# Kernel tuning notes

Hardware: AMD Instinct MI355X
Metric: run time of the kernel (lower is better)

Reference implementation:

```python
import jax, jax.numpy as jnp
import numpy as np

K = 512
DIM = 256
BETA = 0.25


def setup_inputs() -> dict:
    key = jax.random.key(0)
    k1, k2 = jax.random.split(key)
    x = jax.random.normal(k1, (64, DIM, 32, 32), dtype=jnp.float32)
    lookup_table = jax.random.normal(k2, (K, DIM), dtype=jnp.float32)
    return {"x": x, "lookup_table": lookup_table}


def reference(x, lookup_table):
    b, d, h, w = x.shape
    # [b,d,h,w] -> [b*h*w, d]
    xf = jnp.transpose(x, (0, 2, 3, 1)).reshape(-1, d)
    # Squared Euclidean distances (argmin identical to torch.cdist argmin)
    d2 = (
        jnp.sum(xf * xf, axis=-1, keepdims=True)
        - 2.0 * (xf @ lookup_table.T)
        + jnp.sum(lookup_table * lookup_table, axis=-1)
    )  # [N, K]
    q = jnp.argmin(d2, axis=1)  # [N]
    x_e = lookup_table[q].reshape(b, h, w, d).transpose(0, 3, 1, 2)  # [b,d,h,w]
    q_x = q.reshape(b, h, w)
    codebook_loss = jnp.mean(jnp.square(jax.lax.stop_gradient(x) - x_e))
    commitment_loss = jnp.mean(jnp.square(x - jax.lax.stop_gradient(x_e)))
    loss = codebook_loss + BETA * commitment_loss
    return x_e, q_x, loss
```

## Files before the change

kernel.cpp:

```cpp
#include <hip/hip_runtime.h>

#define DIM     256
#define HW      1024
#define N_ROWS  65536
#define NT      512
#define QBM     128
#define NBLK    512
#define MARGIN  0.0625f

#define OUT_Q_OFF    16777216
#define OUT_LOSS_OFF 16842752

#define WS_DIST   512
#define WS_X2     1024
#define WS_CNT_I  1536
#define WS_LIST_I 2048
#define WS_LUTBF_B 524288

typedef __attribute__((ext_vector_type(8))) short short8v;
typedef __attribute__((ext_vector_type(4))) float floatx4;

__device__ __forceinline__ unsigned short bf16_rne(float f) {
    unsigned int u = __float_as_uint(f);
    u += 0x7fffu + ((u >> 16) & 1u);
    return (unsigned short)(u >> 16);
}
__device__ __forceinline__ float bf16_to_f(unsigned short h) {
    return __uint_as_float(((unsigned int)h) << 16);
}
__device__ __forceinline__ uint4 pack8(const unsigned short* h) {
    uint4 u;
    u.x = (unsigned)h[0] | ((unsigned)h[1] << 16);
    u.y = (unsigned)h[2] | ((unsigned)h[3] << 16);
    u.z = (unsigned)h[4] | ((unsigned)h[5] << 16);
    u.w = (unsigned)h[6] | ((unsigned)h[7] << 16);
    return u;
}

__global__ void c2_kernel(const float* __restrict__ lut, float* __restrict__ ws) {
    if (threadIdx.x == 0) ((int*)ws)[WS_CNT_I] = 0;
    int t = threadIdx.x;
    for (int k = t; k < 512; k += 256) {
        const float4* row = (const float4*)(lut + (size_t)k * DIM);
        float s = 0.f;
        #pragma unroll 8
        for (int i = 0; i < DIM / 4; ++i) {
            float4 v = row[i];
            s += v.x * v.x + v.y * v.y + v.z * v.z + v.w * v.w;
        }
        ws[k] = s;
    }
}

__global__ void lutprep_kernel(const float* __restrict__ lut, float* __restrict__ ws) {
    int g = blockIdx.x * 256 + threadIdx.x;
    int lane = g & 63;
    int ctg  = (g >> 6) & 31;
    int dcg  = g >> 11;
    int code = ctg * 16 + (lane & 15);
    int d0   = dcg * 32 + (lane >> 4) * 8;
    const float* src = lut + (size_t)code * DIM + d0;
    unsigned short hi[8], lo[8];
    #pragma unroll
    for (int j = 0; j < 8; ++j) {
        float v = src[j];
        unsigned short h = bf16_rne(v);
        hi[j] = h;
        lo[j] = bf16_rne(v - bf16_to_f(h));
    }
    char* dst = (char*)ws + WS_LUTBF_B + (size_t)((dcg * 32 + ctg) * 2) * 1024 + lane * 16;
    *(uint4*)dst          = pack8(hi);
    *(uint4*)(dst + 1024) = pack8(lo);
}

__global__ __launch_bounds__(NT, 2) void vq_kernel(const float* __restrict__ x,
                                                   const float* __restrict__ lut,
                                                   float* __restrict__ out,
                                                   float* __restrict__ ws) {
    __shared__ char aS[2][16384];
    __shared__ float c2s[512];
    __shared__ float redv1[4][QBM];
    __shared__ float redv2[4][QBM];
    __shared__ int   redi1[4][QBM];
    __shared__ int   qsh[QBM];
    __shared__ float wsumd[2];
    __shared__ float wsumx[8];

    const char* lutbf = (const char*)ws + WS_LUTBF_B;

    const int tid = threadIdx.x;
    const int blk = blockIdx.x;
    const int n0  = blk * QBM;
    const int b   = n0 >> 10;
    const int hw0 = n0 & 1023;
    const float* xb = x + (size_t)b * (DIM * HW) + hw0;

    for (int k = tid; k < 512; k += NT) c2s[k] = ws[k];

    const int wave = tid >> 6;
    const int lane = tid & 63;
    const int l15  = lane & 15;
    const int l4   = lane >> 4;
    const int rg   = wave >> 2;
    const int cg   = wave & 3;

    const int srow   = tid & 127;
    const int schunk = tid >> 7;
    const int srt    = srow >> 4;
    const int slf    = schunk * 16 + (srow & 15);
    char* awr_hi0 = &aS[0][srt * 1024 + slf * 16];
    char* awr_hi1 = &aS[1][srt * 1024 + slf * 16];

    float x2local = 0.f;
    floatx4 acc[4][8];
    #pragma unroll
    for (int i = 0; i < 4; ++i)
        #pragma unroll
        for (int j = 0; j < 8; ++j) acc[i][j] = (floatx4)0.f;

    {
        const float* src = xb + (size_t)(schunk * 8) * HW + srow;
        unsigned short hi[8], lo[8];
        #pragma unroll
        for (int j = 0; j < 8; ++j) {
            float v = src[(size_t)j * HW];
            x2local = fmaf(v, v, x2local);
            unsigned short h = bf16_rne(v);
            hi[j] = h;
            lo[j] = bf16_rne(v - bf16_to_f(h));
        }
        *(uint4*)awr_hi0          = pack8(hi);
        *(uint4*)(awr_hi0 + 8192) = pack8(lo);
    }
    __syncthreads();

    for (int dc = 0; dc < 8; ++dc) {
        const int cur = dc & 1;
        float xn[8];
        if (dc < 7) {
            const float* src = xb + (size_t)((dc + 1) * 32 + schunk * 8) * HW + srow;
            #pragma unroll
            for (int j = 0; j < 8; ++j) xn[j] = src[(size_t)j * HW];
        }
        short8v ah[4], al[4];
        #pragma unroll
        for (int rtl = 0; rtl < 4; ++rtl) {
            const char* ra = &aS[cur][(rg * 4 + rtl) * 1024 + lane * 16];
            ah[rtl] = *(const short8v*)ra;
            al[rtl] = *(const short8v*)(ra + 8192);
        }
        short8v bh[8], bl[8];
        #pragma unroll
        for (int ct = 0; ct < 8; ++ct) {
            const char* bp = lutbf + (size_t)((dc * 32 + cg * 8 + ct) * 2) * 1024 + lane * 16;
            bh[ct] = *(const short8v*)bp;
            bl[ct] = *(const short8v*)(bp + 1024);
        }
        #pragma unroll
        for (int ct = 0; ct < 8; ++ct) {
            #pragma unroll
            for (int rtl = 0; rtl < 4; ++rtl) {
                acc[rtl][ct] = __builtin_amdgcn_mfma_f32_16x16x32_bf16(ah[rtl], bh[ct], acc[rtl][ct], 0, 0, 0);
                acc[rtl][ct] = __builtin_amdgcn_mfma_f32_16x16x32_bf16(al[rtl], bh[ct], acc[rtl][ct], 0, 0, 0);
                acc[rtl][ct] = __builtin_amdgcn_mfma_f32_16x16x32_bf16(ah[rtl], bl[ct], acc[rtl][ct], 0, 0, 0);
            }
        }
        if (dc < 7) {
            unsigned short hi[8], lo[8];
            #pragma unroll
            for (int j = 0; j < 8; ++j) {
                float v = xn[j];
                x2local = fmaf(v, v, x2local);
                unsigned short h = bf16_rne(v);
                hi[j] = h;
                lo[j] = bf16_rne(v - bf16_to_f(h));
            }
            char* wr = cur ? awr_hi0 : awr_hi1;
            *(uint4*)wr          = pack8(hi);
            *(uint4*)(wr + 8192) = pack8(lo);
            __syncthreads();
        }
    }

    #pragma unroll
    for (int rtl = 0; rtl < 4; ++rtl) {
        #pragma unroll
        for (int r = 0; r < 4; ++r) {
            float v1 = 3.4e38f, v2 = 3.4e38f; int i1 = 0;
            #pragma unroll
            for (int ct = 0; ct < 8; ++ct) {
                int code = cg * 128 + ct * 16 + l15;
                float dist = fmaf(-2.f, acc[rtl][ct][r], c2s[code]);
                if (dist < v1) { v2 = v1; v1 = dist; i1 = code; }
                else if (dist < v2) v2 = dist;
            }
            #pragma unroll
            for (int off = 1; off < 16; off <<= 1) {
                float ov1 = __shfl_xor(v1, off, 64);
                int   oi1 = __shfl_xor(i1, off, 64);
                float ov2 = __shfl_xor(v2, off, 64);
                float nv2 = fminf(fmaxf(v1, ov1), fminf(v2, ov2));
                if (ov1 < v1 || (ov1 == v1 && oi1 < i1)) { v1 = ov1; i1 = oi1; }
                v2 = nv2;
            }
            if (l15 == 0) {
                int row = rg * 64 + rtl * 16 + l4 * 4 + r;
                redv1[cg][row] = v1; redi1[cg][row] = i1; redv2[cg][row] = v2;
            }
        }
    }
    __syncthreads();

    float dist_part = 0.f;
    if (tid < QBM) {
        const int row = tid;
        float v1 = redv1[0][row]; int i1 = redi1[0][row]; float v2 = redv2[0][row];
        #pragma unroll
        for (int s = 1; s < 4; ++s) {
            float ov1 = redv1[s][row]; int oi1 = redi1[s][row]; float ov2 = redv2[s][row];
            float nv2 = fminf(fmaxf(v1, ov1), fminf(v2, ov2));
            if (ov1 < v1 || (ov1 == v1 && oi1 < i1)) { v1 = ov1; i1 = oi1; }
            v2 = nv2;
        }
        qsh[row] = i1;
        out[OUT_Q_OFF + n0 + row] = (float)i1;
        if (v2 - v1 <= MARGIN) {
            int idx = atomicAdd((int*)ws + WS_CNT_I, 1);
            ((int*)ws)[WS_LIST_I + idx] = n0 + row;
        }
        dist_part = v1;
    }

    float dv = dist_part;
    #pragma unroll
    for (int off = 32; off; off >>= 1) dv += __shfl_down(dv, off, 64);
    if (lane == 0 && wave < 2) wsumd[wave] = dv;
    float xv = x2local;
    #pragma unroll
    for (int off = 32; off; off >>= 1) xv += __shfl_down(xv, off, 64);
    if (lane == 0) wsumx[wave] = xv;
    __syncthreads();
    if (tid == 0) {
        float xs = 0.f;
        #pragma unroll
        for (int w = 0; w < 8; ++w) xs += wsumx[w];
        ws[WS_DIST + blk] = wsumd[0] + wsumd[1];
        ws[WS_X2 + blk]   = xs;
    }

    {
        const int row = tid & 127;
        const int dg  = tid >> 7;
        const int q   = qsh[row];
        const float* crow = lut + (size_t)q * DIM;
        float* ob = out + (size_t)b * (DIM * HW) + hw0 + row;
        #pragma unroll 4
        for (int i = 0; i < 16; ++i) {
            int d0 = dg * 64 + i * 4;
            float4 c = *(const float4*)(crow + d0);
            ob[(size_t)(d0 + 0) * HW] = c.x;
            ob[(size_t)(d0 + 1) * HW] = c.y;
            ob[(size_t)(d0 + 2) * HW] = c.z;
            ob[(size_t)(d0 + 3) * HW] = c.w;
        }
    }
}

__global__ void exact_kernel(const float* __restrict__ x, const float* __restrict__ lut,
                             float* __restrict__ out, const float* __restrict__ ws) {
    __shared__ float xr[DIM];
    __shared__ float rv[256];
    __shared__ int   ri[256];
    const int cnt = ((const int*)ws)[WS_CNT_I];
    const int* list = (const int*)ws + WS_LIST_I;
    const int tid = threadIdx.x;
    for (int ii = blockIdx.x; ii < cnt; ii += gridDim.x) {
        const int row = list[ii];
        const int b = row >> 10, hw = row & 1023;
        __syncthreads();
        xr[tid] = x[(size_t)b * (DIM * HW) + (size_t)tid * HW + hw];
        __syncthreads();
        float bv = 3.4e38f; int bi = 0;
        #pragma unroll
        for (int k2 = 0; k2 < 2; ++k2) {
            int k = tid + k2 * 256;
            const float* cr = lut + (size_t)k * DIM;
            float dot = 0.f;
            for (int d = 0; d < DIM; ++d) dot = fmaf(xr[d], cr[d], dot);
            float dist = fmaf(-2.f, dot, ws[k]);
            if (dist < bv || (dist == bv && k < bi)) { bv = dist; bi = k; }
        }
        rv[tid] = bv; ri[tid] = bi;
        __syncthreads();
        for (int s = 128; s; s >>= 1) {
            if (tid < s) {
                float ov = rv[tid + s]; int oi = ri[tid + s];
                if (ov < rv[tid] || (ov == rv[tid] && oi < ri[tid])) {
                    rv[tid] = ov; ri[tid] = oi;
                }
            }
            __syncthreads();
        }
        const int q = ri[0];
        if (tid == 0) out[OUT_Q_OFF + row] = (float)q;
        out[(size_t)b * (DIM * HW) + (size_t)tid * HW + hw] = lut[(size_t)q * DIM + tid];
    }
}

__global__ void loss_kernel(float* __restrict__ out, const float* __restrict__ ws) {
    __shared__ float wsum[4];
    int tid = threadIdx.x;
    float s = 0.f;
    for (int i = tid; i < 1024; i += 256) s += ws[WS_DIST + i];
    #pragma unroll
    for (int off = 32; off; off >>= 1) s += __shfl_down(s, off, 64);
    if ((tid & 63) == 0) wsum[tid >> 6] = s;
    __syncthreads();
    if (tid == 0) {
        float total = wsum[0] + wsum[1] + wsum[2] + wsum[3];
        out[OUT_LOSS_OFF] = total * (1.25f / 16777216.f);
    }
}

extern "C" void kernel_launch(void* const* d_in, const int* in_sizes, int n_in,
                              void* d_out, int out_size, void* d_ws, size_t ws_size,
                              hipStream_t stream) {
    const float* x   = (const float*)d_in[0];
    const float* lut = (const float*)d_in[1];
    float* out = (float*)d_out;
    float* ws  = (float*)d_ws;

    c2_kernel<<<1, 256, 0, stream>>>(lut, ws);
    lutprep_kernel<<<64, 256, 0, stream>>>(lut, ws);
    vq_kernel<<<NBLK, NT, 0, stream>>>(x, lut, out, ws);
    exact_kernel<<<2048, 256, 0, stream>>>(x, lut, out, ws);
    loss_kernel<<<1, 256, 0, stream>>>(out, ws);
}
```

Baseline: 147.4 us.

## Stage bf16 codebook tiles in LDS via async global-to-LDS double buffering

The split hi/lo bf16 codebook slices are now copied into a double-buffered 64KB-per-stage LDS region with global_load_lds, prefetching the next d-chunk while the current one is consumed, instead of every wave reading its B fragments straight from global memory. The x tile drops to a single buffer guarded by an extra barrier. The codebook squared norms move from shared memory into registers, and the MFMA loop is reordered into three passes. The cost is 144KB of dynamic LDS per block, which likely allows only one block per CU despite launch bounds asking for two, so latency hiding from occupancy is traded for shared reuse of B across row groups.

Result: no change. 145.6 us (-1.2%).

```diff
diff --git a/kernel.cpp b/kernel.cpp
--- a/kernel.cpp
+++ b/kernel.cpp
@@ -17,8 +17,14 @@
 #define WS_LIST_I 2048
 #define WS_LUTBF_B 524288
 
+#define VQ_LDS (147456)
+
 typedef __attribute__((ext_vector_type(8))) short short8v;
 typedef __attribute__((ext_vector_type(4))) float floatx4;
+
+#define GLOAD_LDS16(gaddr, laddr) \
+    __builtin_amdgcn_global_load_lds((const __attribute__((address_space(1))) unsigned int*)(gaddr), \
+                                     (__attribute__((address_space(3))) unsigned int*)(laddr), 16, 0, 0)
 
 __device__ __forceinline__ unsigned short bf16_rne(float f) {
     unsigned int u = __float_as_uint(f);
@@ -77,14 +83,8 @@
                                                    const float* __restrict__ lut,
                                                    float* __restrict__ out,
                                                    float* __restrict__ ws) {
-    __shared__ char aS[2][16384];
-    __shared__ float c2s[512];
-    __shared__ float redv1[4][QBM];
-    __shared__ float redv2[4][QBM];
-    __shared__ int   redi1[4][QBM];
-    __shared__ int   qsh[QBM];
-    __shared__ float wsumd[2];
-    __shared__ float wsumx[8];
+    extern __shared__ char smem[];
+    char* abuf = smem + 131072;
 
     const char* lutbf = (const char*)ws + WS_LUTBF_B;
 
@@ -95,8 +95,6 @@
     const int hw0 = n0 & 1023;
     const float* xb = x + (size_t)b * (DIM * HW) + hw0;
 
-    for (int k = tid; k < 512; k += NT) c2s[k] = ws[k];
-
     const int wave = tid >> 6;
     const int lane = tid & 63;
     const int l15  = lane & 15;
@@ -104,12 +102,15 @@
     const int rg   = wave >> 2;
     const int cg   = wave & 3;
 
+    float c2reg[8];
+    #pragma unroll
+    for (int ct = 0; ct < 8; ++ct) c2reg[ct] = ws[cg * 128 + ct * 16 + l15];
+
     const int srow   = tid & 127;
     const int schunk = tid >> 7;
     const int srt    = srow >> 4;
     const int slf    = schunk * 16 + (srow & 15);
-    char* awr_hi0 = &aS[0][srt * 1024 + slf * 16];
-    char* awr_hi1 = &aS[1][srt * 1024 + slf * 16];
+    char* awr = abuf + srt * 1024 + slf * 16;
 
     float x2local = 0.f;
     floatx4 acc[4][8];
@@ -119,6 +120,11 @@
         for (int j = 0; j < 8; ++j) acc[i][j] = (floatx4)0.f;
 
     {
+        #pragma unroll
+        for (int c = 0; c < 8; ++c) {
+            int u = c * 8 + wave;
+            GLOAD_LDS16(lutbf + (size_t)u * 1024 + lane * 16, smem + u * 1024);
+        }
         const float* src = xb + (size_t)(schunk * 8) * HW + srow;
         unsigned short hi[8], lo[8];
         #pragma unroll
@@ -129,15 +135,23 @@
             hi[j] = h;
             lo[j] = bf16_rne(v - bf16_to_f(h));
         }
-        *(uint4*)awr_hi0          = pack8(hi);
-        *(uint4*)(awr_hi0 + 8192) = pack8(lo);
+        *(uint4*)awr          = pack8(hi);
+        *(uint4*)(awr + 8192) = pack8(lo);
     }
     __syncthreads();
 
     for (int dc = 0; dc < 8; ++dc) {
         const int cur = dc & 1;
+        char* bcur = smem + cur * 65536;
         float xn[8];
         if (dc < 7) {
+            char* bnxt = smem + (cur ^ 1) * 65536;
+            const char* bsrc = lutbf + (size_t)(dc + 1) * 65536;
+            #pragma unroll
+            for (int c = 0; c < 8; ++c) {
+                int u = c * 8 + wave;
+                GLOAD_LDS16(bsrc + (size_t)u * 1024 + lane * 16, bnxt + u * 1024);
+            }
             const float* src = xb + (size_t)((dc + 1) * 32 + schunk * 8) * HW + srow;
             #pragma unroll
             for (int j = 0; j < 8; ++j) xn[j] = src[(size_t)j * HW];
@@ -145,27 +159,34 @@
         short8v ah[4], al[4];
         #pragma unroll
         for (int rtl = 0; rtl < 4; ++rtl) {
-            const char* ra = &aS[cur][(rg * 4 + rtl) * 1024 + lane * 16];
+            const char* ra = abuf + (rg * 4 + rtl) * 1024 + lane * 16;
             ah[rtl] = *(const short8v*)ra;
             al[rtl] = *(const short8v*)(ra + 8192);
         }
         short8v bh[8], bl[8];
         #pragma unroll
         for (int ct = 0; ct < 8; ++ct) {
-            const char* bp = lutbf + (size_t)((dc * 32 + cg * 8 + ct) * 2) * 1024 + lane * 16;
+            const char* bp = bcur + (size_t)((cg * 8 + ct) * 2) * 1024 + lane * 16;
             bh[ct] = *(const short8v*)bp;
             bl[ct] = *(const short8v*)(bp + 1024);
         }
         #pragma unroll
-        for (int ct = 0; ct < 8; ++ct) {
-            #pragma unroll
-            for (int rtl = 0; rtl < 4; ++rtl) {
+        for (int ct = 0; ct < 8; ++ct)
+            #pragma unroll
+            for (int rtl = 0; rtl < 4; ++rtl)
                 acc[rtl][ct] = __builtin_amdgcn_mfma_f32_16x16x32_bf16(ah[rtl], bh[ct], acc[rtl][ct], 0, 0, 0);
+        #pragma unroll
+        for (int ct = 0; ct < 8; ++ct)
+            #pragma unroll
+            for (int rtl = 0; rtl < 4; ++rtl)
                 acc[rtl][ct] = __builtin_amdgcn_mfma_f32_16x16x32_bf16(al[rtl], bh[ct], acc[rtl][ct], 0, 0, 0);
+        #pragma unroll
+        for (int ct = 0; ct < 8; ++ct)
+            #pragma unroll
+            for (int rtl = 0; rtl < 4; ++rtl)
                 acc[rtl][ct] = __builtin_amdgcn_mfma_f32_16x16x32_bf16(ah[rtl], bl[ct], acc[rtl][ct], 0, 0, 0);
-            }
-        }
         if (dc < 7) {
+            __builtin_amdgcn_s_barrier();
             unsigned short hi[8], lo[8];
             #pragma unroll
             for (int j = 0; j < 8; ++j) {
@@ -175,12 +196,19 @@
                 hi[j] = h;
                 lo[j] = bf16_rne(v - bf16_to_f(h));
             }
-            char* wr = cur ? awr_hi0 : awr_hi1;
-            *(uint4*)wr          = pack8(hi);
-            *(uint4*)(wr + 8192) = pack8(lo);
+            *(uint4*)awr          = pack8(hi);
+            *(uint4*)(awr + 8192) = pack8(lo);
             __syncthreads();
         }
     }
+    __syncthreads();
+
+    float (*redv1)[QBM] = (float (*)[QBM])(abuf);
+    float (*redv2)[QBM] = (float (*)[QBM])(abuf + 2048);
+    int   (*redi1)[QBM] = (int (*)[QBM])(abuf + 4096);
+    int*   qsh   = (int*)(abuf + 6144);
+    float* wsumd = (float*)(abuf + 6656);
+    float* wsumx = (float*)(abuf + 6688);
 
     #pragma unroll
     for (int rtl = 0; rtl < 4; ++rtl) {
@@ -190,7 +218,7 @@
             #pragma unroll
             for (int ct = 0; ct < 8; ++ct) {
                 int code = cg * 128 + ct * 16 + l15;
-                float dist = fmaf(-2.f, acc[rtl][ct][r], c2s[code]);
+                float dist = fmaf(-2.f, acc[rtl][ct][r], c2reg[ct]);
                 if (dist < v1) { v2 = v1; v1 = dist; i1 = code; }
                 else if (dist < v2) v2 = dist;
             }
@@ -330,9 +358,12 @@
     float* out = (float*)d_out;
     float* ws  = (float*)d_ws;
 
+    (void)hipFuncSetAttribute((const void*)vq_kernel,
+                              hipFuncAttributeMaxDynamicSharedMemorySize, VQ_LDS);
+
     c2_kernel<<<1, 256, 0, stream>>>(lut, ws);
     lutprep_kernel<<<64, 256, 0, stream>>>(lut, ws);
-    vq_kernel<<<NBLK, NT, 0, stream>>>(x, lut, out, ws);
+    vq_kernel<<<NBLK, NT, VQ_LDS, stream>>>(x, lut, out, ws);
     exact_kernel<<<2048, 256, 0, stream>>>(x, lut, out, ws);
     loss_kernel<<<1, 256, 0, stream>>>(out, ws);
 }
```
